# Kernel tuning notes

Hardware: AMD Instinct MI355X
Metric: run time of the kernel (lower is better)

## Reference

```python
import jax, jax.numpy as jnp
import numpy as np

B, T, D, H, O = 1024, 512, 64, 64, 32


def setup_inputs() -> dict:
    key = jax.random.key(0)
    ks = jax.random.split(key, 12)
    s = 1.0 / np.sqrt(H)  # torch LSTM/Linear default init scale
    u = lambda k, shape: jax.random.uniform(k, shape, jnp.float32, -s, s)
    return {
        "x": jax.random.normal(ks[0], (B, T, D), jnp.float32),
        # layer 0 (PyTorch gate order: i, f, g, o stacked along first dim)
        "w_ih0": u(ks[1], (4 * H, D)),
        "w_hh0": u(ks[2], (4 * H, H)),
        "b_ih0": u(ks[3], (4 * H,)),
        "b_hh0": u(ks[4], (4 * H,)),
        # layer 1
        "w_ih1": u(ks[5], (4 * H, H)),
        "w_hh1": u(ks[6], (4 * H, H)),
        "b_ih1": u(ks[7], (4 * H,)),
        "b_hh1": u(ks[8], (4 * H,)),
        # final linear head
        "fc_w": u(ks[9], (O, H)),
        "fc_b": u(ks[10], (O,)),
    }


def lstm_layer(x, w_ih, w_hh, b_ih, b_hh):
    """Single batch-first LSTM layer, PyTorch gate order (i, f, g, o)."""
    Bb = x.shape[0]
    Hh = w_hh.shape[1]
    # precompute input contribution for all timesteps: (B, T, 4H)
    pre = jnp.einsum('btd,gd->btg', x, w_ih) + b_ih + b_hh

    def step(carry, p_t):  # p_t: (B, 4H)
        h, c = carry
        gates = p_t + h @ w_hh.T
        i, f, g, o = jnp.split(gates, 4, axis=-1)
        c = jax.nn.sigmoid(f) * c + jax.nn.sigmoid(i) * jnp.tanh(g)
        h = jax.nn.sigmoid(o) * jnp.tanh(c)
        return (h, c), h

    h0 = jnp.zeros((Bb, Hh), x.dtype)
    (_, _), hs = jax.lax.scan(step, (h0, h0), jnp.swapaxes(pre, 0, 1))
    return jnp.swapaxes(hs, 0, 1)  # (B, T, H)


def reference(x, w_ih0, w_hh0, b_ih0, b_hh0, w_ih1, w_hh1, b_ih1, b_hh1, fc_w, fc_b):
    h1 = lstm_layer(x, w_ih0, w_hh0, b_ih0, b_hh0)
    h2 = lstm_layer(h1, w_ih1, w_hh1, b_ih1, b_hh1)
    last = h2[:, -1, :]  # (B, H)
    return jax.nn.softplus(last @ fc_w.T + fc_b)  # (B, O)
```

## Files before the change

### kernel.cpp

```cpp
#include <hip/hip_runtime.h>
#include <math.h>

#define BB 1024
#define TT 512
#define OO 32
#define MM 4
#define NBLK (BB/MM)

typedef __attribute__((ext_vector_type(8))) short short8;
typedef __attribute__((ext_vector_type(4))) float f32x4;

#define MFMA __builtin_amdgcn_mfma_f32_16x16x32_bf16
#define LOG2E 1.4426950408889634f
#define K2    2.8853900817779268f

#define BAR() asm volatile("s_waitcnt lgkmcnt(0)\n\ts_barrier" ::: "memory")

__device__ __forceinline__ float exp2f_(float x) {
#if __has_builtin(__builtin_amdgcn_exp2f)
    return __builtin_amdgcn_exp2f(x);
#else
    float r; asm("v_exp_f32 %0, %1" : "=v"(r) : "v"(x)); return r;
#endif
}

__device__ __forceinline__ ushort f2bf(float f) {
    union { float f; unsigned u; } v; v.f = f;
    unsigned r = v.u + 0x7FFF + ((v.u >> 16) & 1);
    return (ushort)(r >> 16);
}
__device__ __forceinline__ float bf2f(ushort u) {
    union { unsigned u; float f; } v; v.u = ((unsigned)u) << 16; return v.f;
}
__device__ __forceinline__ unsigned pkbf(float a, float b) {
    union { float f; unsigned u; } x, y; x.f = a; y.f = b;
    return __builtin_amdgcn_perm(y.u + 0x8000u, x.u + 0x8000u, 0x07060302u);
}
__device__ __forceinline__ short8 pack8(const float4& a, const float4& b) {
    union { unsigned u[4]; short8 s; } r;
    r.u[0] = pkbf(a.x, a.y); r.u[1] = pkbf(a.z, a.w);
    r.u[2] = pkbf(b.x, b.y); r.u[3] = pkbf(b.z, b.w);
    return r.s;
}

__global__ __launch_bounds__(512)
void lstm_f256(const float* __restrict__ x,
               const float* __restrict__ w_ih0,
               const float* __restrict__ w_hh0,
               const float* __restrict__ b_ih0,
               const float* __restrict__ b_hh0,
               const float* __restrict__ w_ih1,
               const float* __restrict__ w_hh1,
               const float* __restrict__ b_ih1,
               const float* __restrict__ b_hh1,
               const float* __restrict__ fc_w,
               const float* __restrict__ fc_b,
               float* __restrict__ out)
{
    __shared__ __align__(16) ushort h0s[2][4][80];
    __shared__ __align__(16) ushort h1s[2][4][80];

    const int tid  = threadIdx.x;
    const int wv   = tid >> 6;
    const bool gB  = (wv >= 4);
    const int u    = wv & 3;
    const int ln   = tid & 63;
    const int l15  = ln & 15;
    const int quad = ln >> 4;
    const int b0   = blockIdx.x * MM;
    const int hq   = 16 * u + l15;
    const int xr   = l15 >> 2;

    const float* wih = gB ? w_ih1 : w_ih0;
    const float* whh = gB ? w_hh1 : w_hh0;
    const float* bih = gB ? b_ih1 : b_ih0;
    const float* bhh = gB ? b_hh1 : b_hh0;

    short8 bfrag[4][4];
    f32x4  bias4[4];
#pragma unroll
    for (int g = 0; g < 4; ++g) {
        const float sc = (g == 2) ? K2 : -LOG2E;
        const int col = 64 * g + 16 * u + l15;
        const float bv = (bih[col] + bhh[col]) * sc;
        bias4[g] = (f32x4){bv, bv, bv, bv};
#pragma unroll
        for (int kt = 0; kt < 4; ++kt) {
            const int kb = kt * 32 + quad * 8;
            const float* src = (kb < 64) ? (wih + col * 64 + kb)
                                         : (whh + col * 64 + (kb - 64));
            const float4 v0 = *(const float4*)src;
            const float4 v1 = *(const float4*)(src + 4);
            short8 b;
            b[0] = (short)f2bf(v0.x * sc); b[1] = (short)f2bf(v0.y * sc);
            b[2] = (short)f2bf(v0.z * sc); b[3] = (short)f2bf(v0.w * sc);
            b[4] = (short)f2bf(v1.x * sc); b[5] = (short)f2bf(v1.y * sc);
            b[6] = (short)f2bf(v1.z * sc); b[7] = (short)f2bf(v1.w * sc);
            bfrag[g][kt] = b;
        }
    }

    const size_t xoff = ((size_t)(b0 + xr) * TT) * 64 + quad * 8;
    float4 xfA0, xfA1, xfA2, xfA3, xfB0, xfB1, xfB2, xfB3;
    f32x4 pre[4];
    const f32x4 z4 = (f32x4){0.f, 0.f, 0.f, 0.f};

#define ISSUE(t_, S)                                                          \
    if ((t_) < TT) {                                                          \
        const float* p = x + xoff + (size_t)(t_) * 64;                        \
        xf##S##0 = *(const float4*)p;        xf##S##1 = *(const float4*)(p + 4);  \
        xf##S##2 = *(const float4*)(p + 32); xf##S##3 = *(const float4*)(p + 36); \
    }

    for (int i = tid; i < 2 * 4 * 80; i += 512) {
        ((ushort*)h0s)[i] = 0;
        ((ushort*)h1s)[i] = 0;
    }

    float cc = 0.f;
    if (!gB) {
        ISSUE(0, A);
        ISSUE(1, B);
        const short8 xlo = pack8(xfA0, xfA1);
        const short8 xhi = pack8(xfA2, xfA3);
#pragma unroll
        for (int g = 0; g < 4; ++g)
            pre[g] = MFMA(xhi, bfrag[g][1],
                          MFMA(xlo, bfrag[g][0], bias4[g], 0, 0, 0), 0, 0, 0);
    }
    BAR();

#define CELL1(YI, YF, YG, YO, HD, NXT)                                        \
    {                                                                         \
        const float Ef = exp2f_(YF);                                          \
        const float Ei = exp2f_(YI);                                          \
        const float Eg = exp2f_(fminf((YG), 80.f));                           \
        const float sf = __builtin_amdgcn_rcpf(1.f + Ef);                     \
        const float rd = __builtin_amdgcn_rcpf((1.f + Ei) * (1.f + Eg));      \
        cc = sf * cc + (Eg - 1.f) * rd;                                       \
        const float Ec = exp2f_(fminf(cc * K2, 80.f));                        \
        const float Eo = exp2f_(YO);                                          \
        const float r2 = __builtin_amdgcn_rcpf((1.f + Eo) * (1.f + Ec));      \
        union { float f; unsigned uu; } hv; hv.f = (Ec - 1.f) * r2;           \
        HD[NXT][quad][hq] = (ushort)((hv.uu + 0x8000u) >> 16);                \
    }

#define STEP(t_, CUR, NXT, USE, LD, DOA, DOB)                                 \
    {                                                                         \
        if (!gB) {                                                            \
            if (DOA) {                                                        \
                const short8 a2 = *(const short8*)&h0s[CUR][xr][quad * 8];    \
                const short8 a3 = *(const short8*)&h0s[CUR][xr][32 + quad * 8]; \
                f32x4 aA[4], aB[4];                                           \
                _Pragma("unroll")                                             \
                for (int g = 0; g < 4; ++g) {                                 \
                    aA[g] = MFMA(a2, bfrag[g][2], pre[g], 0, 0, 0);           \
                    aB[g] = MFMA(a3, bfrag[g][3], z4, 0, 0, 0);               \
                }                                                             \
                ISSUE((t_) + 2, LD);                                          \
                const float yi = aA[0][0] + aB[0][0];                         \
                const float yf = aA[1][0] + aB[1][0];                         \
                const float yg = aA[2][0] + aB[2][0];                         \
                const float yo = aA[3][0] + aB[3][0];                         \
                CELL1(yi, yf, yg, yo, h0s, NXT);                              \
                if ((t_) + 1 < TT) {                                          \
                    const short8 xlo = pack8(xf##USE##0, xf##USE##1);         \
                    const short8 xhi = pack8(xf##USE##2, xf##USE##3);         \
                    _Pragma("unroll")                                         \
                    for (int g = 0; g < 4; ++g)                               \
                        pre[g] = MFMA(xhi, bfrag[g][1],                       \
                                      MFMA(xlo, bfrag[g][0], bias4[g], 0,0,0), 0,0,0); \
                }                                                             \
            }                                                                 \
        } else {                                                              \
            if (DOB) {                                                        \
                const short8 a0 = *(const short8*)&h0s[CUR][xr][quad * 8];    \
                const short8 a1 = *(const short8*)&h0s[CUR][xr][32 + quad * 8]; \
                const short8 a2 = *(const short8*)&h1s[CUR][xr][quad * 8];    \
                const short8 a3 = *(const short8*)&h1s[CUR][xr][32 + quad * 8]; \
                f32x4 aA[4], aB[4];                                           \
                _Pragma("unroll")                                             \
                for (int g = 0; g < 4; ++g) {                                 \
                    aA[g] = MFMA(a1, bfrag[g][1],                             \
                                 MFMA(a0, bfrag[g][0], bias4[g], 0, 0, 0), 0, 0, 0); \
                    aB[g] = MFMA(a3, bfrag[g][3],                             \
                                 MFMA(a2, bfrag[g][2], z4, 0, 0, 0), 0, 0, 0); \
                }                                                             \
                const float yi = aA[0][0] + aB[0][0];                         \
                const float yf = aA[1][0] + aB[1][0];                         \
                const float yg = aA[2][0] + aB[2][0];                         \
                const float yo = aA[3][0] + aB[3][0];                         \
                CELL1(yi, yf, yg, yo, h1s, NXT);                              \
            }                                                                 \
        }                                                                     \
        BAR();                                                                \
    }

    STEP(0, 0, 1, B, A, 1, 0)
    for (int tb = 1; tb + 2 < TT; tb += 2) {
        STEP(tb,     1, 0, A, B, 1, 1)
        STEP(tb + 1, 0, 1, B, A, 1, 1)
    }
    STEP(TT - 1, 1, 0, A, B, 1, 1)
    STEP(TT, 0, 1, B, A, 0, 1)
#undef STEP
#undef CELL1
#undef ISSUE

    if (tid < MM * OO) {
        const int row = tid >> 5, o = tid & 31;
        float a = fc_b[o];
#pragma unroll
        for (int j = 0; j < 64; ++j)
            a = fmaf(fc_w[o * 64 + j], bf2f(h1s[1][row][j]), a);
        out[(size_t)(b0 + row) * OO + o] =
            fmaxf(a, 0.0f) + log1pf(__expf(-fabsf(a)));
    }
}

extern "C" void kernel_launch(void* const* d_in, const int* in_sizes, int n_in,
                              void* d_out, int out_size, void* d_ws, size_t ws_size,
                              hipStream_t stream) {
    const float* x     = (const float*)d_in[0];
    const float* w_ih0 = (const float*)d_in[1];
    const float* w_hh0 = (const float*)d_in[2];
    const float* b_ih0 = (const float*)d_in[3];
    const float* b_hh0 = (const float*)d_in[4];
    const float* w_ih1 = (const float*)d_in[5];
    const float* w_hh1 = (const float*)d_in[6];
    const float* b_ih1 = (const float*)d_in[7];
    const float* b_hh1 = (const float*)d_in[8];
    const float* fc_w  = (const float*)d_in[9];
    const float* fc_b  = (const float*)d_in[10];
    float* out = (float*)d_out;

    lstm_f256<<<dim3(NBLK), dim3(512), 0, stream>>>(
        x, w_ih0, w_hh0, b_ih0, b_hh0,
        w_ih1, w_hh1, b_ih1, b_hh1, fc_w, fc_b, out);
}
```

Measured before the change: 485.3 us.

## Restructure LSTM into 4-step super-steps with cooperative input projections

Replaces the per-timestep kernel with a super-step loop where each of 128 iterations processes 4 timesteps. All 8 waves cooperatively compute the input projections for layer 0 (from x) and layer 1 (from the previous super-step's layer-0 outputs) into shared memory. Each wave then runs only the recurrent MFMAs for one batch row across 4 timesteps. This cuts block-wide barriers from about one per timestep to two per 4 timesteps and moves input-projection work off the serial critical path. In exchange it adds redundant recurrent MFMAs (all 4 column tiles are computed per wave and only one is kept), larger shared buffers with swizzling, and a launch bound requesting 2 blocks per CU.

```diff
diff --git a/kernel.cpp b/kernel.cpp
--- a/kernel.cpp
+++ b/kernel.cpp
@@ -6,6 +6,7 @@
 #define OO 32
 #define MM 4
 #define NBLK (BB/MM)
+#define NSUP 128
 
 typedef __attribute__((ext_vector_type(8))) short short8;
 typedef __attribute__((ext_vector_type(4))) float f32x4;
@@ -43,176 +44,216 @@
     return r.s;
 }
 
-__global__ __launch_bounds__(512)
-void lstm_f256(const float* __restrict__ x,
-               const float* __restrict__ w_ih0,
-               const float* __restrict__ w_hh0,
-               const float* __restrict__ b_ih0,
-               const float* __restrict__ b_hh0,
-               const float* __restrict__ w_ih1,
-               const float* __restrict__ w_hh1,
-               const float* __restrict__ b_ih1,
-               const float* __restrict__ b_hh1,
-               const float* __restrict__ fc_w,
-               const float* __restrict__ fc_b,
-               float* __restrict__ out)
+__global__ __launch_bounds__(512, 2)
+void lstm_rw(const float* __restrict__ x,
+             const float* __restrict__ w_ih0,
+             const float* __restrict__ w_hh0,
+             const float* __restrict__ b_ih0,
+             const float* __restrict__ b_hh0,
+             const float* __restrict__ w_ih1,
+             const float* __restrict__ w_hh1,
+             const float* __restrict__ b_ih1,
+             const float* __restrict__ b_hh1,
+             const float* __restrict__ fc_w,
+             const float* __restrict__ fc_b,
+             float* __restrict__ out)
 {
-    __shared__ __align__(16) ushort h0s[2][4][80];
-    __shared__ __align__(16) ushort h1s[2][4][80];
+    __shared__ float  pre0r[2][4][4][4][64];
+    __shared__ float  pre1r[2][4][4][4][64];
+    __shared__ ushort h0r[2][16][64];
+    __shared__ ushort h1b[2][4][64];
 
     const int tid  = threadIdx.x;
     const int wv   = tid >> 6;
     const bool gB  = (wv >= 4);
-    const int u    = wv & 3;
+    const int r    = wv & 3;
     const int ln   = tid & 63;
     const int l15  = ln & 15;
     const int quad = ln >> 4;
     const int b0   = blockIdx.x * MM;
-    const int hq   = 16 * u + l15;
-    const int xr   = l15 >> 2;
-
-    const float* wih = gB ? w_ih1 : w_ih0;
+    const int hq   = 16 * quad + l15;
+
     const float* whh = gB ? w_hh1 : w_hh0;
-    const float* bih = gB ? b_ih1 : b_ih0;
-    const float* bhh = gB ? b_hh1 : b_hh0;
-
-    short8 bfrag[4][4];
-    f32x4  bias4[4];
+    short8 bf[4][4][2];
 #pragma unroll
     for (int g = 0; g < 4; ++g) {
         const float sc = (g == 2) ? K2 : -LOG2E;
-        const int col = 64 * g + 16 * u + l15;
-        const float bv = (bih[col] + bhh[col]) * sc;
-        bias4[g] = (f32x4){bv, bv, bv, bv};
-#pragma unroll
-        for (int kt = 0; kt < 4; ++kt) {
-            const int kb = kt * 32 + quad * 8;
-            const float* src = (kb < 64) ? (wih + col * 64 + kb)
-                                         : (whh + col * 64 + (kb - 64));
-            const float4 v0 = *(const float4*)src;
-            const float4 v1 = *(const float4*)(src + 4);
-            short8 b;
-            b[0] = (short)f2bf(v0.x * sc); b[1] = (short)f2bf(v0.y * sc);
-            b[2] = (short)f2bf(v0.z * sc); b[3] = (short)f2bf(v0.w * sc);
-            b[4] = (short)f2bf(v1.x * sc); b[5] = (short)f2bf(v1.y * sc);
-            b[6] = (short)f2bf(v1.z * sc); b[7] = (short)f2bf(v1.w * sc);
-            bfrag[g][kt] = b;
-        }
-    }
-
-    const size_t xoff = ((size_t)(b0 + xr) * TT) * 64 + quad * 8;
-    float4 xfA0, xfA1, xfA2, xfA3, xfB0, xfB1, xfB2, xfB3;
-    f32x4 pre[4];
+#pragma unroll
+        for (int c = 0; c < 4; ++c) {
+            const int col = 64 * g + 16 * c + l15;
+#pragma unroll
+            for (int kt = 0; kt < 2; ++kt) {
+                const float* src = whh + col * 64 + 32 * kt + 8 * quad;
+                const float4 v0 = *(const float4*)src;
+                const float4 v1 = *(const float4*)(src + 4);
+                short8 b;
+                b[0] = (short)f2bf(v0.x * sc); b[1] = (short)f2bf(v0.y * sc);
+                b[2] = (short)f2bf(v0.z * sc); b[3] = (short)f2bf(v0.w * sc);
+                b[4] = (short)f2bf(v1.x * sc); b[5] = (short)f2bf(v1.y * sc);
+                b[6] = (short)f2bf(v1.z * sc); b[7] = (short)f2bf(v1.w * sc);
+                bf[g][c][kt] = b;
+            }
+        }
+    }
+
+    const int tiA = 2 * wv, tiB = 2 * wv + 1;
+    const int gA_ = tiA >> 2, cA_ = tiA & 3;
+    const int gB_ = tiB >> 2, cB_ = tiB & 3;
+    short8 wi0A[2], wi0B[2], wi1A[2], wi1B[2];
+    float bias0A, bias0B, bias1A, bias1B;
+    {
+        const float scA = (gA_ == 2) ? K2 : -LOG2E;
+        const float scB = (gB_ == 2) ? K2 : -LOG2E;
+        const int colA = 64 * gA_ + 16 * cA_ + l15;
+        const int colB = 64 * gB_ + 16 * cB_ + l15;
+        bias0A = (b_ih0[colA] + b_hh0[colA]) * scA;
+        bias0B = (b_ih0[colB] + b_hh0[colB]) * scB;
+        bias1A = (b_ih1[colA] + b_hh1[colA]) * scA;
+        bias1B = (b_ih1[colB] + b_hh1[colB]) * scB;
+#pragma unroll
+        for (int kt = 0; kt < 2; ++kt) {
+            const int ko = 32 * kt + 8 * quad;
+#define LDW(dst, W, col, sc)                                                  \
+            { const float4 v0 = *(const float4*)(W + (col) * 64 + ko);        \
+              const float4 v1 = *(const float4*)(W + (col) * 64 + ko + 4);    \
+              short8 b;                                                       \
+              b[0]=(short)f2bf(v0.x*(sc)); b[1]=(short)f2bf(v0.y*(sc));       \
+              b[2]=(short)f2bf(v0.z*(sc)); b[3]=(short)f2bf(v0.w*(sc));       \
+              b[4]=(short)f2bf(v1.x*(sc)); b[5]=(short)f2bf(v1.y*(sc));       \
+              b[6]=(short)f2bf(v1.z*(sc)); b[7]=(short)f2bf(v1.w*(sc));       \
+              dst = b; }
+            LDW(wi0A[kt], w_ih0, colA, scA)
+            LDW(wi0B[kt], w_ih0, colB, scB)
+            LDW(wi1A[kt], w_ih1, colA, scA)
+            LDW(wi1B[kt], w_ih1, colB, scB)
+#undef LDW
+        }
+    }
+
+    for (int i = tid; i < 2 * 16 * 64; i += 512) ((ushort*)h0r)[i] = 0;
+    for (int i = tid; i < 2 * 4 * 64; i += 512) ((ushort*)h1b)[i] = 0;
+
+    const int xrr = l15 & 3, xtt = l15 >> 2;
+    const size_t xbase = ((size_t)(b0 + xrr) * TT) * 64 + 8 * quad;
+    float4 xp0, xp1, xp2, xp3;
+    {
+        const float* p = x + xbase + (size_t)xtt * 64;
+        xp0 = *(const float4*)p;        xp1 = *(const float4*)(p + 4);
+        xp2 = *(const float4*)(p + 32); xp3 = *(const float4*)(p + 36);
+    }
+
+    float cc = 0.f;
     const f32x4 z4 = (f32x4){0.f, 0.f, 0.f, 0.f};
 
-#define ISSUE(t_, S)                                                          \
-    if ((t_) < TT) {                                                          \
-        const float* p = x + xoff + (size_t)(t_) * 64;                        \
-        xf##S##0 = *(const float4*)p;        xf##S##1 = *(const float4*)(p + 4);  \
-        xf##S##2 = *(const float4*)(p + 32); xf##S##3 = *(const float4*)(p + 36); \
-    }
-
-    for (int i = tid; i < 2 * 4 * 80; i += 512) {
-        ((ushort*)h0s)[i] = 0;
-        ((ushort*)h1s)[i] = 0;
-    }
-
-    float cc = 0.f;
-    if (!gB) {
-        ISSUE(0, A);
-        ISSUE(1, B);
-        const short8 xlo = pack8(xfA0, xfA1);
-        const short8 xhi = pack8(xfA2, xfA3);
-#pragma unroll
-        for (int g = 0; g < 4; ++g)
-            pre[g] = MFMA(xhi, bfrag[g][1],
-                          MFMA(xlo, bfrag[g][0], bias4[g], 0, 0, 0), 0, 0, 0);
-    }
+#define CELLH(LVAL)                                                           \
+    {                                                                         \
+        const float Ef = exp2f_(y1);                                         \
+        const float Ei = exp2f_(y0);                                         \
+        const float Eg = exp2f_(fminf(y2, 80.f));                            \
+        const float sf = __builtin_amdgcn_rcpf(1.f + Ef);                    \
+        const float rd = __builtin_amdgcn_rcpf((1.f + Ei) * (1.f + Eg));     \
+        cc = sf * cc + (Eg - 1.f) * rd;                                      \
+        const float Ec = exp2f_(fminf(cc * K2, 80.f));                       \
+        const float Eo = exp2f_(y3);                                         \
+        const float r2 = __builtin_amdgcn_rcpf((1.f + Eo) * (1.f + Ec));     \
+        union { float f; unsigned u; } hv; hv.f = (Ec - 1.f) * r2;           \
+        LVAL = (ushort)((hv.u + 0x8000u) >> 16);                             \
+    }
+
+#define RECUR(aa0, aa1)                                                       \
+    _Pragma("unroll")                                                         \
+    for (int c = 0; c < 4; ++c) {                                             \
+        f32x4 A0 = MFMA(aa0, bf[0][c][0], z4, 0,0,0);                         \
+        A0 = MFMA(aa1, bf[0][c][1], A0, 0,0,0);                               \
+        f32x4 A1 = MFMA(aa0, bf[1][c][0], z4, 0,0,0);                         \
+        A1 = MFMA(aa1, bf[1][c][1], A1, 0,0,0);                               \
+        f32x4 A2 = MFMA(aa0, bf[2][c][0], z4, 0,0,0);                         \
+        A2 = MFMA(aa1, bf[2][c][1], A2, 0,0,0);                               \
+        f32x4 A3 = MFMA(aa0, bf[3][c][0], z4, 0,0,0);                         \
+        A3 = MFMA(aa1, bf[3][c][1], A3, 0,0,0);                               \
+        if (quad == c) { y0 += A0[0]; y1 += A1[0]; y2 += A2[0]; y3 += A3[0]; }\
+    }
+
+#define COOPTILE(DST, A0_, A1_, W_, BV, G_, C_)                               \
+    {                                                                         \
+        f32x4 a = (f32x4){BV, BV, BV, BV};                                    \
+        a = MFMA(A0_, W_[0], a, 0,0,0);                                       \
+        a = MFMA(A1_, W_[1], a, 0,0,0);                                       \
+        float* dst = &DST[cb][quad][0][G_][16 * (C_) + l15];                  \
+        dst[0] = a[0]; dst[256] = a[1]; dst[512] = a[2]; dst[768] = a[3];     \
+    }
+
+    for (int s = 0; s <= NSUP; ++s) {
+        BAR();
+        const int cb = s & 1, pb = cb ^ 1;
+
+        if (s < NSUP) {
+            const short8 xlo = pack8(xp0, xp1);
+            const short8 xhi = pack8(xp2, xp3);
+            COOPTILE(pre0r, xlo, xhi, wi0A, bias0A, gA_, cA_)
+            COOPTILE(pre0r, xlo, xhi, wi0B, bias0B, gB_, cB_)
+        }
+        if (s >= 1) {
+            const char* hb = (const char*)&h0r[pb][0][0];
+            const int sw = (l15 & 7) << 4;
+            const short8 hA0 = *(const short8*)(hb + l15 * 128 + ((16 * quad) ^ sw));
+            const short8 hA1 = *(const short8*)(hb + l15 * 128 + ((64 + 16 * quad) ^ sw));
+            COOPTILE(pre1r, hA0, hA1, wi1A, bias1A, gA_, cA_)
+            COOPTILE(pre1r, hA0, hA1, wi1B, bias1B, gB_, cB_)
+        }
+        if (s + 1 < NSUP) {
+            const float* p = x + xbase + (size_t)(4 * (s + 1) + xtt) * 64;
+            xp0 = *(const float4*)p;        xp1 = *(const float4*)(p + 4);
+            xp2 = *(const float4*)(p + 32); xp3 = *(const float4*)(p + 36);
+        }
+        BAR();
+
+        if (!gB) {
+            if (s < NSUP) {
+#pragma unroll
+                for (int tau = 0; tau < 4; ++tau) {
+                    const int rb = (tau == 0) ? pb : cb;
+                    const int m  = (tau == 0) ? (12 + r) : (4 * (tau - 1) + r);
+                    const char* hb = (const char*)&h0r[rb][0][0];
+                    const int sw = (m & 7) << 4;
+                    const short8 a0 = *(const short8*)(hb + m * 128 + ((16 * quad) ^ sw));
+                    const short8 a1 = *(const short8*)(hb + m * 128 + ((64 + 16 * quad) ^ sw));
+                    const float* pp = &pre0r[cb][tau][r][0][hq];
+                    float y0 = pp[0], y1 = pp[64], y2 = pp[128], y3 = pp[192];
+                    RECUR(a0, a1)
+                    const int mo = 4 * tau + r;
+                    ushort hval; CELLH(hval)
+                    *(ushort*)((char*)&h0r[cb][0][0] + mo * 128 +
+                               ((2 * hq) ^ ((mo & 7) << 4))) = hval;
+                }
+            }
+        } else {
+            if (s >= 1) {
+#pragma unroll
+                for (int tau = 0; tau < 4; ++tau) {
+                    const char* hb = (const char*)&h1b[(tau + 1) & 1][r][0];
+                    const short8 a0 = *(const short8*)(hb + 16 * quad);
+                    const short8 a1 = *(const short8*)(hb + 64 + 16 * quad);
+                    const float* pp = &pre1r[cb][tau][r][0][hq];
+                    float y0 = pp[0], y1 = pp[64], y2 = pp[128], y3 = pp[192];
+                    RECUR(a0, a1)
+                    ushort hval; CELLH(hval)
+                    h1b[tau & 1][r][hq] = hval;
+                }
+            }
+        }
+    }
+#undef COOPTILE
+#undef RECUR
+#undef CELLH
+
     BAR();
-
-#define CELL1(YI, YF, YG, YO, HD, NXT)                                        \
-    {                                                                         \
-        const float Ef = exp2f_(YF);                                          \
-        const float Ei = exp2f_(YI);                                          \
-        const float Eg = exp2f_(fminf((YG), 80.f));                           \
-        const float sf = __builtin_amdgcn_rcpf(1.f + Ef);                     \
-        const float rd = __builtin_amdgcn_rcpf((1.f + Ei) * (1.f + Eg));      \
-        cc = sf * cc + (Eg - 1.f) * rd;                                       \
-        const float Ec = exp2f_(fminf(cc * K2, 80.f));                        \
-        const float Eo = exp2f_(YO);                                          \
-        const float r2 = __builtin_amdgcn_rcpf((1.f + Eo) * (1.f + Ec));      \
-        union { float f; unsigned uu; } hv; hv.f = (Ec - 1.f) * r2;           \
-        HD[NXT][quad][hq] = (ushort)((hv.uu + 0x8000u) >> 16);                \
-    }
-
-#define STEP(t_, CUR, NXT, USE, LD, DOA, DOB)                                 \
-    {                                                                         \
-        if (!gB) {                                                            \
-            if (DOA) {                                                        \
-                const short8 a2 = *(const short8*)&h0s[CUR][xr][quad * 8];    \
-                const short8 a3 = *(const short8*)&h0s[CUR][xr][32 + quad * 8]; \
-                f32x4 aA[4], aB[4];                                           \
-                _Pragma("unroll")                                             \
-                for (int g = 0; g < 4; ++g) {                                 \
-                    aA[g] = MFMA(a2, bfrag[g][2], pre[g], 0, 0, 0);           \
-                    aB[g] = MFMA(a3, bfrag[g][3], z4, 0, 0, 0);               \
-                }                                                             \
-                ISSUE((t_) + 2, LD);                                          \
-                const float yi = aA[0][0] + aB[0][0];                         \
-                const float yf = aA[1][0] + aB[1][0];                         \
-                const float yg = aA[2][0] + aB[2][0];                         \
-                const float yo = aA[3][0] + aB[3][0];                         \
-                CELL1(yi, yf, yg, yo, h0s, NXT);                              \
-                if ((t_) + 1 < TT) {                                          \
-                    const short8 xlo = pack8(xf##USE##0, xf##USE##1);         \
-                    const short8 xhi = pack8(xf##USE##2, xf##USE##3);         \
-                    _Pragma("unroll")                                         \
-                    for (int g = 0; g < 4; ++g)                               \
-                        pre[g] = MFMA(xhi, bfrag[g][1],                       \
-                                      MFMA(xlo, bfrag[g][0], bias4[g], 0,0,0), 0,0,0); \
-                }                                                             \
-            }                                                                 \
-        } else {                                                              \
-            if (DOB) {                                                        \
-                const short8 a0 = *(const short8*)&h0s[CUR][xr][quad * 8];    \
-                const short8 a1 = *(const short8*)&h0s[CUR][xr][32 + quad * 8]; \
-                const short8 a2 = *(const short8*)&h1s[CUR][xr][quad * 8];    \
-                const short8 a3 = *(const short8*)&h1s[CUR][xr][32 + quad * 8]; \
-                f32x4 aA[4], aB[4];                                           \
-                _Pragma("unroll")                                             \
-                for (int g = 0; g < 4; ++g) {                                 \
-                    aA[g] = MFMA(a1, bfrag[g][1],                             \
-                                 MFMA(a0, bfrag[g][0], bias4[g], 0, 0, 0), 0, 0, 0); \
-                    aB[g] = MFMA(a3, bfrag[g][3],                             \
-                                 MFMA(a2, bfrag[g][2], z4, 0, 0, 0), 0, 0, 0); \
-                }                                                             \
-                const float yi = aA[0][0] + aB[0][0];                         \
-                const float yf = aA[1][0] + aB[1][0];                         \
-                const float yg = aA[2][0] + aB[2][0];                         \
-                const float yo = aA[3][0] + aB[3][0];                         \
-                CELL1(yi, yf, yg, yo, h1s, NXT);                              \
-            }                                                                 \
-        }                                                                     \
-        BAR();                                                                \
-    }
-
-    STEP(0, 0, 1, B, A, 1, 0)
-    for (int tb = 1; tb + 2 < TT; tb += 2) {
-        STEP(tb,     1, 0, A, B, 1, 1)
-        STEP(tb + 1, 0, 1, B, A, 1, 1)
-    }
-    STEP(TT - 1, 1, 0, A, B, 1, 1)
-    STEP(TT, 0, 1, B, A, 0, 1)
-#undef STEP
-#undef CELL1
-#undef ISSUE
-
     if (tid < MM * OO) {
         const int row = tid >> 5, o = tid & 31;
         float a = fc_b[o];
 #pragma unroll
         for (int j = 0; j < 64; ++j)
-            a = fmaf(fc_w[o * 64 + j], bf2f(h1s[1][row][j]), a);
+            a = fmaf(fc_w[o * 64 + j], bf2f(h1b[1][row][j]), a);
         out[(size_t)(b0 + row) * OO + o] =
             fmaxf(a, 0.0f) + log1pf(__expf(-fabsf(a)));
     }
@@ -234,7 +275,7 @@
     const float* fc_b  = (const float*)d_in[10];
     float* out = (float*)d_out;
 
-    lstm_f256<<<dim3(NBLK), dim3(512), 0, stream>>>(
+    lstm_rw<<<dim3(NBLK), dim3(512), 0, stream>>>(
         x, w_ih0, w_hh0, b_ih0, b_hh0,
         w_ih1, w_hh1, b_ih1, b_hh1, fc_w, fc_b, out);
 }
```

After: 682.0 us. +40.5%, slower.
